# Performance work log

Hardware: AMD Instinct MI355X
Metric: run time of the kernel (lower is better)

The kernel has to match this reference:

```python
import jax, jax.numpy as jnp
import numpy as np

N, H, W, C = 4, 128, 128, 128
G = 8
GC = C // G
K = 9  # 3x3 deformable kernel
PAD = 1
HIN, WIN = H + 2 * PAD, W + 2 * PAD
EPS = 1e-5
OFFSET_SCALE = 1.0


def ln(x, g, b):
    m = jnp.mean(x, -1, keepdims=True)
    v = jnp.mean((x - m) ** 2, -1, keepdims=True)
    return (x - m) * jax.lax.rsqrt(v + EPS) * g + b


def gelu(x):
    return jax.nn.gelu(x, approximate=False)


def dcn_core(xp, offset, mask):
    # xp: (N,H,W,C) value features; offset: (N,H,W,G*K*2); mask: (N,H,W,G,K)
    xpad = jnp.pad(xp, ((0, 0), (PAD, PAD), (PAD, PAD), (0, 0)))
    img = xpad.reshape(N, HIN * WIN, G, GC)
    # reference points normalized by padded size (matches dcnv3_core_pytorch)
    ref_x = (jnp.arange(W, dtype=jnp.float32) + 1.5) / WIN  # (dil*(k-1))//2 + 0.5
    ref_y = (jnp.arange(H, dtype=jnp.float32) + 1.5) / HIN
    RX, RY = jnp.meshgrid(ref_x, ref_y)  # (H,W), xy indexing
    ref = jnp.stack([RX, RY], -1)  # (H,W,2) as (x,y)
    gx, gy = jnp.meshgrid(jnp.linspace(-1.0, 1.0, 3), jnp.linspace(-1.0, 1.0, 3), indexing='ij')
    grid = jnp.stack([gx / WIN, gy / HIN], -1).reshape(K, 2)  # dilation grid, x-major
    off = offset.reshape(N, H, W, G, K, 2)
    loc = (ref[None, :, :, None, None, :] + grid * OFFSET_SCALE
           + off * OFFSET_SCALE / jnp.array([WIN, HIN], jnp.float32))  # (N,H,W,G,K,2)
    # grid_sample align_corners=False pixel coords
    px = loc[..., 0] * WIN - 0.5
    py = loc[..., 1] * HIN - 0.5
    x0 = jnp.floor(px); y0 = jnp.floor(py)
    tx = px - x0; ty = py - y0
    x0i = x0.astype(jnp.int32); y0i = y0.astype(jnp.int32)
    x1i = x0i + 1; y1i = y0i + 1

    def gather(iy, ix):
        valid = ((iy >= 0) & (iy < HIN) & (ix >= 0) & (ix < WIN)).astype(xp.dtype)
        idx = jnp.clip(iy, 0, HIN - 1) * WIN + jnp.clip(ix, 0, WIN - 1)  # (N,H,W,G,K)
        idxf = idx.transpose(0, 1, 2, 4, 3).reshape(N, H * W * K, G, 1)
        v = jnp.take_along_axis(img, idxf, axis=1).reshape(N, H, W, K, G, GC)
        return v * valid.transpose(0, 1, 2, 4, 3)[..., None]

    acc = jnp.zeros((N, H, W, G, GC), xp.dtype)
    for iy, ix, wgt in ((y0i, x0i, (1 - ty) * (1 - tx)),
                        (y0i, x1i, (1 - ty) * tx),
                        (y1i, x0i, ty * (1 - tx)),
                        (y1i, x1i, ty * tx)):
        wm = (wgt * mask).transpose(0, 1, 2, 4, 3)[..., None]  # (N,H,W,K,G,1)
        acc = acc + jnp.sum(gather(iy, ix) * wm, axis=3)  # (N,H,W,G,GC)
    return acc.reshape(N, H, W, C)


def dcn(x, in_w, in_b, dw_k, dw_b, dwln_g, dwln_b, off_w, off_b, mask_w, mask_b, out_w, out_b):
    xp = x @ in_w + in_b  # input_proj
    # offset/mask branch: depthwise 3x3 conv on raw input, LN, GELU
    xc = jax.lax.conv_general_dilated(
        x, dw_k.reshape(3, 3, 1, C), (1, 1), 'SAME',
        dimension_numbers=('NHWC', 'HWIO', 'NHWC'), feature_group_count=C) + dw_b
    x1 = gelu(ln(xc, dwln_g, dwln_b))
    offset = x1 @ off_w + off_b  # (N,H,W,G*K*2)
    mask = jax.nn.softmax((x1 @ mask_w + mask_b).reshape(N, H, W, G, K), axis=-1)
    y = dcn_core(xp, offset, mask)
    return y @ out_w + out_b


def _forward(x, ln1_g, ln1_b, in_w, in_b, dw_k, dw_b, dwln_g, dwln_b, off_w, off_b,
             mask_w, mask_b, out_w, out_b, ln2_g, ln2_b, fc1_w, fc1_b, fc2_w, fc2_b):
    # pre-norm, no layer_scale, no drop_path (rate 0)
    x = x + dcn(ln(x, ln1_g, ln1_b), in_w, in_b, dw_k, dw_b, dwln_g, dwln_b,
                off_w, off_b, mask_w, mask_b, out_w, out_b)
    h = ln(x, ln2_g, ln2_b)
    h = gelu(h @ fc1_w + fc1_b) @ fc2_w + fc2_b
    return x + h


def setup_inputs() -> dict:
    key = jax.random.key(0)
    ks = jax.random.split(key, 10)

    def lin(k, fin, fout, scale=1.0):
        s = scale / np.sqrt(fin)
        return jax.random.uniform(k, (fin, fout), minval=-s, maxval=s, dtype=jnp.float32)

    d = {}
    d['x'] = jax.random.normal(ks[0], (N, H, W, C), dtype=jnp.float32)
    d['ln1_g'] = jnp.ones((C,), jnp.float32); d['ln1_b'] = jnp.zeros((C,), jnp.float32)
    d['in_w'] = lin(ks[1], C, C); d['in_b'] = jnp.zeros((C,), jnp.float32)
    d['dw_k'] = jax.random.normal(ks[2], (3, 3, C), dtype=jnp.float32) * 0.05
    d['dw_b'] = jnp.zeros((C,), jnp.float32)
    d['dwln_g'] = jnp.ones((C,), jnp.float32); d['dwln_b'] = jnp.zeros((C,), jnp.float32)
    d['off_w'] = lin(ks[3], C, G * K * 2, 0.1); d['off_b'] = jnp.zeros((G * K * 2,), jnp.float32)
    d['mask_w'] = lin(ks[4], C, G * K, 0.1); d['mask_b'] = jnp.zeros((G * K,), jnp.float32)
    d['out_w'] = lin(ks[5], C, C); d['out_b'] = jnp.zeros((C,), jnp.float32)
    d['ln2_g'] = jnp.ones((C,), jnp.float32); d['ln2_b'] = jnp.zeros((C,), jnp.float32)
    d['fc1_w'] = lin(ks[6], C, 4 * C); d['fc1_b'] = jnp.zeros((4 * C,), jnp.float32)
    d['fc2_w'] = lin(ks[7], 4 * C, C); d['fc2_b'] = jnp.zeros((C,), jnp.float32)
    return d


def reference(x, ln1_g, ln1_b, in_w, in_b, dw_k, dw_b, dwln_g, dwln_b, off_w, off_b,
              mask_w, mask_b, out_w, out_b, ln2_g, ln2_b, fc1_w, fc1_b, fc2_w, fc2_b):
    return _forward(x, ln1_g, ln1_b, in_w, in_b, dw_k, dw_b, dwln_g, dwln_b, off_w, off_b,
                    mask_w, mask_b, out_w, out_b, ln2_g, ln2_b, fc1_w, fc1_b, fc2_w, fc2_b)
```

## Files before the change

kernel.cpp:

```cpp
#include <hip/hip_runtime.h>
#include <hip/hip_bf16.h>
#include <math.h>

#define NB 4
#define HH 128
#define WW 128
#define CC 128
#define GG 8
#define GCC 16
#define KK 9
#define NHW (NB*HH*WW)

typedef __hip_bfloat16 bf16;
typedef __attribute__((ext_vector_type(8))) short short8;
typedef __attribute__((ext_vector_type(4))) float f32x4;

__device__ __forceinline__ float b2f(bf16 v){ return __bfloat162float(v); }
__device__ __forceinline__ bf16 f2b(float v){ return __float2bfloat16(v); }
__device__ __forceinline__ float gelu_f(float v){ return 0.5f*v*(1.f+erff(v*0.70710678118654752f)); }
__device__ __forceinline__ float lo_bf(unsigned u){ union{unsigned i; float f;} c; c.i = u<<16; return c.f; }
__device__ __forceinline__ float hi_bf(unsigned u){ union{unsigned i; float f;} c; c.i = u&0xffff0000u; return c.f; }
__device__ __forceinline__ unsigned pk(float a, float b){
  return ((unsigned)__bfloat16_as_ushort(f2b(b))<<16) | (unsigned)__bfloat16_as_ushort(f2b(a));
}
__device__ __forceinline__ void st_out(bf16* p, float v){ *p = f2b(v); }
__device__ __forceinline__ void st_out(float* p, float v){ *p = v; }
__device__ __forceinline__ void acc8(float* a, uint4 u, float w){
  a[0]+=w*lo_bf(u.x); a[1]+=w*hi_bf(u.x); a[2]+=w*lo_bf(u.y); a[3]+=w*hi_bf(u.y);
  a[4]+=w*lo_bf(u.z); a[5]+=w*hi_bf(u.z); a[6]+=w*lo_bf(u.w); a[7]+=w*hi_bf(u.w);
}

__global__ __launch_bounds__(256) void prep_k(
    const float* __restrict__ inw,  const float* __restrict__ outw,
    const float* __restrict__ fc1w, const float* __restrict__ fc2w,
    const float* __restrict__ offw, const float* __restrict__ offb,
    const float* __restrict__ maskw,const float* __restrict__ maskb,
    bf16* __restrict__ inwt, bf16* __restrict__ outwt,
    bf16* __restrict__ w1t,  bf16* __restrict__ w2t,
    bf16* __restrict__ wsw,  float* __restrict__ cw)
{
  int idx = blockIdx.x*256 + threadIdx.x;
  if (idx < 16384){
    int n = idx>>7, k = idx&127;
    inwt[idx] = f2b(inw[(size_t)k*128 + n]);
  } else if (idx < 32768){
    int i = idx-16384; int n = i>>7, k = i&127;
    outwt[i] = f2b(outw[(size_t)k*128 + n]);
  } else if (idx < 98304){
    int i = idx-32768; int n = i>>7, k = i&127;
    w1t[i] = f2b(fc1w[(size_t)k*512 + n]);
  } else if (idx < 163840){
    int i = idx-98304; int n = i>>9, k = i&511;
    w2t[i] = f2b(fc2w[(size_t)k*128 + n]);
  } else if (idx < 192512){
    int i = idx-163840; int nn = i>>7, k = i&127;
    float v = (nn<144) ? offw[(size_t)k*144+nn] : (nn<216 ? maskw[(size_t)k*72+(nn-144)] : 0.f);
    wsw[i] = f2b(v);
  } else if (idx < 192736){
    int i = idx-192512;
    cw[i] = (i<144) ? offb[i] : (i<216 ? maskb[i-144] : 0.f);
  }
}

__global__ __launch_bounds__(256) void ln_k(const float* __restrict__ X,
    const float* __restrict__ gam, const float* __restrict__ bet, bf16* __restrict__ Y)
{
  int lane = threadIdx.x & 63;
  int wid  = threadIdx.x >> 6;
  size_t pix = (size_t)blockIdx.x*4 + wid;
  const float* xp = X + pix*CC;
  int c0 = lane*2;
  float v0 = xp[c0], v1 = xp[c0+1];
  float s = v0+v1, ss = v0*v0+v1*v1;
  #pragma unroll
  for (int off=32; off>0; off>>=1){ s += __shfl_xor(s,off,64); ss += __shfl_xor(ss,off,64); }
  float mean = s*(1.f/CC);
  float var  = ss*(1.f/CC) - mean*mean;
  float rstd = rsqrtf(var + 1e-5f);
  float y0 = (v0-mean)*rstd*gam[c0]   + bet[c0];
  float y1 = (v1-mean)*rstd*gam[c0+1] + bet[c0+1];
  Y[pix*CC + c0]   = f2b(y0);
  Y[pix*CC + c0+1] = f2b(y1);
}

__global__ __launch_bounds__(256) void convln_k(const bf16* __restrict__ XN,
    const float* __restrict__ dwk, const float* __restrict__ dwb,
    const float* __restrict__ gam, const float* __restrict__ bet, bf16* __restrict__ X1)
{
  int tid = threadIdx.x;
  int px = tid>>4, cg = tid&15;
  int ch0 = cg*8;
  int pix = blockIdx.x*16 + px;
  int w = pix & (WW-1), h = (pix>>7)&(HH-1), n = pix>>14;
  float acc[8];
  {
    float4 b0 = *(const float4*)(dwb + ch0), b1 = *(const float4*)(dwb + ch0 + 4);
    acc[0]=b0.x; acc[1]=b0.y; acc[2]=b0.z; acc[3]=b0.w;
    acc[4]=b1.x; acc[5]=b1.y; acc[6]=b1.z; acc[7]=b1.w;
  }
  #pragma unroll
  for (int ky=0;ky<3;ky++){
    int yy = h+ky-1; if ((unsigned)yy>=(unsigned)HH) continue;
    #pragma unroll
    for (int kx=0;kx<3;kx++){
      int xx = w+kx-1; if ((unsigned)xx>=(unsigned)WW) continue;
      uint4 u = *(const uint4*)(XN + ((size_t)((n*HH+yy)*WW+xx))*CC + ch0);
      const float* wp = dwk + (ky*3+kx)*CC + ch0;
      float4 w0 = *(const float4*)wp; float4 w1 = *(const float4*)(wp+4);
      acc[0] += lo_bf(u.x)*w0.x; acc[1] += hi_bf(u.x)*w0.y;
      acc[2] += lo_bf(u.y)*w0.z; acc[3] += hi_bf(u.y)*w0.w;
      acc[4] += lo_bf(u.z)*w1.x; acc[5] += hi_bf(u.z)*w1.y;
      acc[6] += lo_bf(u.w)*w1.z; acc[7] += hi_bf(u.w)*w1.w;
    }
  }
  float s=0.f, ss=0.f;
  #pragma unroll
  for (int i=0;i<8;i++){ s += acc[i]; ss += acc[i]*acc[i]; }
  #pragma unroll
  for (int off=1; off<16; off<<=1){ s += __shfl_xor(s,off,64); ss += __shfl_xor(ss,off,64); }
  float mean=s*(1.f/CC), var=ss*(1.f/CC)-mean*mean, rstd=rsqrtf(var+1e-5f);
  float4 g0 = *(const float4*)(gam + ch0), g1 = *(const float4*)(gam + ch0 + 4);
  float4 be0 = *(const float4*)(bet + ch0), be1 = *(const float4*)(bet + ch0 + 4);
  float gv[8] = {g0.x,g0.y,g0.z,g0.w,g1.x,g1.y,g1.z,g1.w};
  float bv[8] = {be0.x,be0.y,be0.z,be0.w,be1.x,be1.y,be1.z,be1.w};
  float o[8];
  #pragma unroll
  for (int i=0;i<8;i++) o[i] = gelu_f((acc[i]-mean)*rstd*gv[i] + bv[i]);
  uint4 up; up.x = pk(o[0],o[1]); up.y = pk(o[2],o[3]); up.z = pk(o[4],o[5]); up.w = pk(o[6],o[7]);
  *(uint4*)(X1 + (size_t)pix*CC + ch0) = up;
}

#define OMS 226
__global__ __launch_bounds__(256) void samp_k(const bf16* __restrict__ X1,
    const bf16* __restrict__ XP,
    const bf16* __restrict__ wsw, const float* __restrict__ cw,
    bf16* __restrict__ Y)
{
  __shared__ bf16 oms[32*OMS];
  int tid = threadIdx.x;
  int pix0 = blockIdx.x*32;
  int wave = tid>>6, l = tid&63, lo16 = l&15, quad = l>>4;
  int nt0 = wave*4;
  int ntn = (wave==3) ? 2 : 4;
  short8 af[2][4];
  #pragma unroll
  for (int mt=0;mt<2;mt++)
    #pragma unroll
    for (int ks=0;ks<4;ks++)
      af[mt][ks] = *(const short8*)(X1 + (size_t)(pix0+mt*16+lo16)*128 + ks*32 + quad*8);
  f32x4 z = {0.f,0.f,0.f,0.f};
  f32x4 acc[2][4];
  #pragma unroll
  for (int mt=0;mt<2;mt++)
    #pragma unroll
    for (int t=0;t<4;t++) acc[mt][t]=z;
  for (int t=0;t<ntn;t++){
    int nt = nt0+t;
    #pragma unroll
    for (int ks=0;ks<4;ks++){
      short8 bfr = *(const short8*)(wsw + (size_t)(nt*16+lo16)*128 + ks*32 + quad*8);
      acc[0][t] = __builtin_amdgcn_mfma_f32_16x16x32_bf16(af[0][ks], bfr, acc[0][t], 0,0,0);
      acc[1][t] = __builtin_amdgcn_mfma_f32_16x16x32_bf16(af[1][ks], bfr, acc[1][t], 0,0,0);
    }
  }
  for (int t=0;t<ntn;t++){
    int col = (nt0+t)*16 + lo16;
    float bb = cw[col];
    #pragma unroll
    for (int mt=0;mt<2;mt++)
      #pragma unroll
      for (int r=0;r<4;r++)
        oms[(mt*16 + quad*4 + r)*OMS + col] = f2b(acc[mt][t][r] + bb);
  }
  __syncthreads();
  {
    int m = tid>>3, g = tid&7;
    int base = m*OMS + 144 + g*9;
    float sc[9]; float mx = -1e30f;
    #pragma unroll
    for (int k=0;k<9;k++){ sc[k] = b2f(oms[base+k]); mx = fmaxf(mx, sc[k]); }
    float sum = 0.f;
    #pragma unroll
    for (int k=0;k<9;k++){ sc[k] = expf(sc[k]-mx); sum += sc[k]; }
    float inv = 1.f/sum;
    #pragma unroll
    for (int k=0;k<9;k++) oms[base+k] = f2b(sc[k]*inv);
  }
  __syncthreads();
  int oct = tid&15, sl = tid>>4;
  int g = oct>>1;
  int ch = g*GCC + (oct&1)*8;
  int w0 = pix0 & (WW-1);
  int h  = (pix0>>7) & (HH-1);
  int n  = pix0>>14;
  const bf16* base = XP + (size_t)n*HH*WW*CC + ch;
  for (int it=0; it<2; it++){
    int m = it*16 + sl;
    int wc = w0 + m;
    const bf16* omrow = &oms[m*OMS];
    float a[8] = {0.f,0.f,0.f,0.f,0.f,0.f,0.f,0.f};
    #pragma unroll
    for (int k=0;k<9;k++){
      float offx = b2f(omrow[g*18 + 2*k]);
      float offy = b2f(omrow[g*18 + 2*k + 1]);
      float mk   = b2f(omrow[144 + g*9 + k]);
      float pxf = (float)(wc + (k/3) - 1) + offx;
      float pyf = (float)(h  + (k%3) - 1) + offy;
      float x0f = floorf(pxf), y0f = floorf(pyf);
      float txf = pxf-x0f,     tyf = pyf-y0f;
      int x0 = (int)x0f, y0 = (int)y0f;
      int x1i = x0+1,    y1i = y0+1;
      float vx0 = ((unsigned)x0 <(unsigned)WW)?1.f:0.f;
      float vx1 = ((unsigned)x1i<(unsigned)WW)?1.f:0.f;
      float vy0 = ((unsigned)y0 <(unsigned)HH)?1.f:0.f;
      float vy1 = ((unsigned)y1i<(unsigned)HH)?1.f:0.f;
      int cx0 = min(max(x0,0),WW-1),  cx1 = min(max(x1i,0),WW-1);
      int cy0 = min(max(y0,0),HH-1),  cy1 = min(max(y1i,0),HH-1);
      float w00=(1.f-tyf)*(1.f-txf)*mk*vy0*vx0, w01=(1.f-tyf)*txf*mk*vy0*vx1;
      float w10=tyf*(1.f-txf)*mk*vy1*vx0,       w11=tyf*txf*mk*vy1*vx1;
      uint4 u00 = *(const uint4*)(base + ((size_t)(cy0*WW+cx0))*CC);
      uint4 u01 = *(const uint4*)(base + ((size_t)(cy0*WW+cx1))*CC);
      uint4 u10 = *(const uint4*)(base + ((size_t)(cy1*WW+cx0))*CC);
      uint4 u11 = *(const uint4*)(base + ((size_t)(cy1*WW+cx1))*CC);
      acc8(a,u00,w00); acc8(a,u01,w01); acc8(a,u10,w10); acc8(a,u11,w11);
    }
    uint4 outp;
    outp.x = pk(a[0],a[1]); outp.y = pk(a[2],a[3]);
    outp.z = pk(a[4],a[5]); outp.w = pk(a[6],a[7]);
    *(uint4*)(Y + (size_t)(pix0+m)*CC + ch) = outp;
  }
}

template<typename OutT, bool RES>
__global__ __launch_bounds__(256) void gemm_mfma(const bf16* __restrict__ A,
    const bf16* __restrict__ Bt, const float* __restrict__ bias,
    const float* __restrict__ res, OutT* __restrict__ C)
{
  int tid = threadIdx.x;
  int wave = tid>>6, l = tid&63, lo16 = l&15, quad = l>>4;
  int m0 = blockIdx.y*256 + wave*64;
  int n0 = blockIdx.x*64;
  short8 bfr[4][4];
  #pragma unroll
  for (int ks=0;ks<4;ks++)
    #pragma unroll
    for (int nt=0;nt<4;nt++)
      bfr[ks][nt] = *(const short8*)(Bt + (size_t)(n0+nt*16+lo16)*128 + ks*32 + quad*8);
  f32x4 z = {0.f,0.f,0.f,0.f};
  f32x4 acc[4][4];
  #pragma unroll
  for (int mt=0;mt<4;mt++)
    #pragma unroll
    for (int nt=0;nt<4;nt++) acc[mt][nt]=z;
  #pragma unroll
  for (int ks=0;ks<4;ks++){
    short8 af[4];
    #pragma unroll
    for (int mt=0;mt<4;mt++)
      af[mt] = *(const short8*)(A + (size_t)(m0+mt*16+lo16)*128 + ks*32 + quad*8);
    #pragma unroll
    for (int nt=0;nt<4;nt++)
      #pragma unroll
      for (int mt=0;mt<4;mt++)
        acc[mt][nt] = __builtin_amdgcn_mfma_f32_16x16x32_bf16(af[mt], bfr[ks][nt], acc[mt][nt], 0,0,0);
  }
  #pragma unroll
  for (int mt=0;mt<4;mt++)
    #pragma unroll
    for (int nt=0;nt<4;nt++){
      int col = n0 + nt*16 + lo16;
      float bb = bias[col];
      #pragma unroll
      for (int r=0;r<4;r++){
        int row = m0 + mt*16 + quad*4 + r;
        float v = acc[mt][nt][r] + bb;
        if (RES) v += res[(size_t)row*128 + col];
        st_out(&C[(size_t)row*128 + col], v);
      }
    }
}

__global__ __launch_bounds__(256) void mlp_mfma(const float* __restrict__ X2,
    const float* __restrict__ lng, const float* __restrict__ lnb,
    const bf16* __restrict__ w1t, const float* __restrict__ b1,
    const bf16* __restrict__ w2t, const float* __restrict__ b2,
    float* __restrict__ OUT)
{
  __shared__ __align__(16) char smem[34816 + 18432];
  bf16* h0s = (bf16*)smem;
  bf16* ts  = (bf16*)smem;
  bf16* w1s = (bf16*)(smem + 34816);
  bf16* w2s = (bf16*)(smem + 34816);
  int tid = threadIdx.x;
  int wave = tid>>6, l = tid&63, lo16 = l&15, quad = l>>4;
  int m0 = blockIdx.x*128;
  #pragma unroll
  for (int itn=0; itn<2; itn++){
    int px = (tid>>2) + itn*64;
    int q = tid&3;
    const float* xr = X2 + (size_t)(m0+px)*128 + q*32;
    float v[32];
    #pragma unroll
    for (int i=0;i<8;i++) *(float4*)(v+i*4) = *(const float4*)(xr+i*4);
    float s=0.f, ss=0.f;
    #pragma unroll
    for (int i=0;i<32;i++){ s += v[i]; ss += v[i]*v[i]; }
    s  += __shfl_xor(s,1,64);  ss += __shfl_xor(ss,1,64);
    s  += __shfl_xor(s,2,64);  ss += __shfl_xor(ss,2,64);
    float mean = s*(1.f/CC), var = ss*(1.f/CC)-mean*mean, rstd = rsqrtf(var+1e-5f);
    const float* gp = lng + q*32; const float* bp = lnb + q*32;
    uint4* dst = (uint4*)(&h0s[px*136 + q*32]);
    #pragma unroll
    for (int i=0;i<4;i++){
      float4 g0 = *(const float4*)(gp+i*8),  g1 = *(const float4*)(gp+i*8+4);
      float4 c0v = *(const float4*)(bp+i*8), c1v = *(const float4*)(bp+i*8+4);
      float o0 = (v[i*8+0]-mean)*rstd*g0.x + c0v.x;
      float o1 = (v[i*8+1]-mean)*rstd*g0.y + c0v.y;
      float o2 = (v[i*8+2]-mean)*rstd*g0.z + c0v.z;
      float o3 = (v[i*8+3]-mean)*rstd*g0.w + c0v.w;
      float o4 = (v[i*8+4]-mean)*rstd*g1.x + c1v.x;
      float o5 = (v[i*8+5]-mean)*rstd*g1.y + c1v.y;
      float o6 = (v[i*8+6]-mean)*rstd*g1.z + c1v.z;
      float o7 = (v[i*8+7]-mean)*rstd*g1.w + c1v.w;
      uint4 up; up.x = pk(o0,o1); up.y = pk(o2,o3); up.z = pk(o4,o5); up.w = pk(o6,o7);
      dst[i] = up;
    }
  }
  __syncthreads();
  short8 a1[2][4];
  #pragma unroll
  for (int mt=0;mt<2;mt++)
    #pragma unroll
    for (int ks=0;ks<4;ks++)
      a1[mt][ks] = *(const short8*)(&h0s[(wave*32 + mt*16 + lo16)*136 + ks*32 + quad*8]);
  f32x4 z = {0.f,0.f,0.f,0.f};
  f32x4 acc2[2][8];
  #pragma unroll
  for (int mt=0;mt<2;mt++)
    #pragma unroll
    for (int nt=0;nt<8;nt++) acc2[mt][nt]=z;

  for (int c0=0;c0<512;c0+=64){
    __syncthreads();
    #pragma unroll
    for (int it=0;it<4;it++){
      int e = it*2048 + tid*8;
      int nn = e>>7, kk = e&127;
      *(uint4*)(&w1s[nn*136 + kk]) = *(const uint4*)(w1t + (size_t)(c0+nn)*128 + kk);
    }
    __syncthreads();
    f32x4 acc1[2][4];
    #pragma unroll
    for (int mt=0;mt<2;mt++)
      #pragma unroll
      for (int nt=0;nt<4;nt++) acc1[mt][nt]=z;
    #pragma unroll
    for (int ks=0;ks<4;ks++)
      #pragma unroll
      for (int nt=0;nt<4;nt++){
        short8 bfr = *(const short8*)(&w1s[(nt*16+lo16)*136 + ks*32 + quad*8]);
        acc1[0][nt] = __builtin_amdgcn_mfma_f32_16x16x32_bf16(a1[0][ks], bfr, acc1[0][nt], 0,0,0);
        acc1[1][nt] = __builtin_amdgcn_mfma_f32_16x16x32_bf16(a1[1][ks], bfr, acc1[1][nt], 0,0,0);
      }
    #pragma unroll
    for (int mt=0;mt<2;mt++)
      #pragma unroll
      for (int nt=0;nt<4;nt++){
        float bb = b1[c0 + nt*16 + lo16];
        #pragma unroll
        for (int r=0;r<4;r++)
          ts[(wave*32 + mt*16 + quad*4 + r)*72 + nt*16 + lo16] = f2b(gelu_f(acc1[mt][nt][r] + bb));
      }
    __syncthreads();
    #pragma unroll
    for (int it=0;it<4;it++){
      int e = it*2048 + tid*8;
      int nn = e>>6, kk = e&63;
      *(uint4*)(&w2s[nn*72 + kk]) = *(const uint4*)(w2t + (size_t)nn*512 + c0 + kk);
    }
    __syncthreads();
    #pragma unroll
    for (int ks2=0;ks2<2;ks2++){
      short8 a2[2];
      #pragma unroll
      for (int mt=0;mt<2;mt++)
        a2[mt] = *(const short8*)(&ts[(wave*32 + mt*16 + lo16)*72 + ks2*32 + quad*8]);
      #pragma unroll
      for (int nt2=0;nt2<8;nt2++){
        short8 bfr2 = *(const short8*)(&w2s[(nt2*16+lo16)*72 + ks2*32 + quad*8]);
        acc2[0][nt2] = __builtin_amdgcn_mfma_f32_16x16x32_bf16(a2[0], bfr2, acc2[0][nt2], 0,0,0);
        acc2[1][nt2] = __builtin_amdgcn_mfma_f32_16x16x32_bf16(a2[1], bfr2, acc2[1][nt2], 0,0,0);
      }
    }
  }
  #pragma unroll
  for (int mt=0;mt<2;mt++)
    #pragma unroll
    for (int nt=0;nt<8;nt++){
      int col = nt*16 + lo16;
      float bb = b2[col];
      #pragma unroll
      for (int r=0;r<4;r++){
        int row = m0 + wave*32 + mt*16 + quad*4 + r;
        float v = acc2[mt][nt][r] + bb + X2[(size_t)row*128 + col];
        OUT[(size_t)row*128 + col] = v;
      }
    }
}

extern "C" void kernel_launch(void* const* d_in, const int* in_sizes, int n_in,
                              void* d_out, int out_size, void* d_ws, size_t ws_size,
                              hipStream_t stream)
{
  const float* x    = (const float*)d_in[0];
  const float* ln1g = (const float*)d_in[1];
  const float* ln1b = (const float*)d_in[2];
  const float* inw  = (const float*)d_in[3];
  const float* inb  = (const float*)d_in[4];
  const float* dwk  = (const float*)d_in[5];
  const float* dwb  = (const float*)d_in[6];
  const float* dwlng= (const float*)d_in[7];
  const float* dwlnb= (const float*)d_in[8];
  const float* offw = (const float*)d_in[9];
  const float* offb = (const float*)d_in[10];
  const float* maskw= (const float*)d_in[11];
  const float* maskb= (const float*)d_in[12];
  const float* outw = (const float*)d_in[13];
  const float* outb = (const float*)d_in[14];
  const float* ln2g = (const float*)d_in[15];
  const float* ln2b = (const float*)d_in[16];
  const float* fc1w = (const float*)d_in[17];
  const float* fc1b = (const float*)d_in[18];
  const float* fc2w = (const float*)d_in[19];
  const float* fc2b = (const float*)d_in[20];
  float* out = (float*)d_out;

  bf16* ws = (bf16*)d_ws;
  const size_t S = (size_t)NHW*CC;
  bf16* xn = ws;
  bf16* xp = ws + S;
  bf16* x1 = ws + 2*S;
  bf16* y  = xn;
  float* x2 = out;
  bf16* inwt  = ws + 3*S;
  bf16* outwt = inwt + 128*128;
  bf16* w1t   = outwt + 128*128;
  bf16* w2t   = w1t + 512*128;
  bf16* wsw   = w2t + 128*512;
  float* cw   = (float*)(wsw + 224*128);

  prep_k<<<753, 256, 0, stream>>>(inw, outw, fc1w, fc2w, offw, offb, maskw, maskb,
                                  inwt, outwt, w1t, w2t, wsw, cw);
  ln_k<<<NHW/4, 256, 0, stream>>>(x, ln1g, ln1b, xn);
  gemm_mfma<bf16,false><<<dim3(2,256), 256, 0, stream>>>(xn, inwt, inb, nullptr, xp);
  convln_k<<<NHW/16, 256, 0, stream>>>(xn, dwk, dwb, dwlng, dwlnb, x1);
  samp_k<<<NHW/32, 256, 0, stream>>>(x1, xp, wsw, cw, y);
  gemm_mfma<float,true><<<dim3(2,256), 256, 0, stream>>>(y, outwt, outb, x, x2);
  mlp_mfma<<<NHW/128, 256, 0, stream>>>(x2, ln2g, ln2b, w1t, fc1b, w2t, fc2b, out);
}
```

Before: 282.8 us.

## Fuse LN1 with input projection; halve MLP tile and merge weight-load barriers

Replaces the separate LayerNorm kernel and input-projection GEMM with one kernel. It normalizes a 64-pixel tile into shared memory, writes the bf16 result to global for the conv path, and runs the MFMA projection from LDS, which removes one launch and a global re-read of xn. The MLP kernel now uses 64-row tiles instead of 128, doubling the grid to 1024 blocks. It also gives fc1 and fc2 weights separate LDS buffers so both load behind a single barrier per chunk. Smaller tiles mean each block reuses the weights it loads across fewer rows, so weight traffic from L2 goes up in exchange for better occupancy and parallelism.

```diff
diff --git a/kernel.cpp b/kernel.cpp
--- a/kernel.cpp
+++ b/kernel.cpp
@@ -62,25 +62,84 @@
   }
 }
 
-__global__ __launch_bounds__(256) void ln_k(const float* __restrict__ X,
-    const float* __restrict__ gam, const float* __restrict__ bet, bf16* __restrict__ Y)
-{
-  int lane = threadIdx.x & 63;
-  int wid  = threadIdx.x >> 6;
-  size_t pix = (size_t)blockIdx.x*4 + wid;
-  const float* xp = X + pix*CC;
-  int c0 = lane*2;
-  float v0 = xp[c0], v1 = xp[c0+1];
-  float s = v0+v1, ss = v0*v0+v1*v1;
-  #pragma unroll
-  for (int off=32; off>0; off>>=1){ s += __shfl_xor(s,off,64); ss += __shfl_xor(ss,off,64); }
-  float mean = s*(1.f/CC);
-  float var  = ss*(1.f/CC) - mean*mean;
-  float rstd = rsqrtf(var + 1e-5f);
-  float y0 = (v0-mean)*rstd*gam[c0]   + bet[c0];
-  float y1 = (v1-mean)*rstd*gam[c0+1] + bet[c0+1];
-  Y[pix*CC + c0]   = f2b(y0);
-  Y[pix*CC + c0+1] = f2b(y1);
+__global__ __launch_bounds__(256) void lnproj_k(const float* __restrict__ X,
+    const float* __restrict__ lng, const float* __restrict__ lnb,
+    const bf16* __restrict__ inwt, const float* __restrict__ inb,
+    bf16* __restrict__ XN, bf16* __restrict__ XP)
+{
+  __shared__ bf16 h0s[64*136];
+  __shared__ bf16 wst[64*136];
+  int tid = threadIdx.x;
+  int wave = tid>>6, l = tid&63, lo16 = l&15, quad = l>>4;
+  int m0 = blockIdx.x*64;
+  {
+    int px = tid>>2, q = tid&3;
+    const float* xr = X + (size_t)(m0+px)*128 + q*32;
+    float v[32];
+    #pragma unroll
+    for (int i=0;i<8;i++) *(float4*)(v+i*4) = *(const float4*)(xr+i*4);
+    float s=0.f, ss=0.f;
+    #pragma unroll
+    for (int i=0;i<32;i++){ s += v[i]; ss += v[i]*v[i]; }
+    s  += __shfl_xor(s,1,64);  ss += __shfl_xor(ss,1,64);
+    s  += __shfl_xor(s,2,64);  ss += __shfl_xor(ss,2,64);
+    float mean = s*(1.f/CC), var = ss*(1.f/CC)-mean*mean, rstd = rsqrtf(var+1e-5f);
+    const float* gp = lng + q*32; const float* bp = lnb + q*32;
+    uint4* dst  = (uint4*)(&h0s[px*136 + q*32]);
+    uint4* dstg = (uint4*)(XN + (size_t)(m0+px)*128 + q*32);
+    #pragma unroll
+    for (int i=0;i<4;i++){
+      float4 g0 = *(const float4*)(gp+i*8),  g1 = *(const float4*)(gp+i*8+4);
+      float4 c0v = *(const float4*)(bp+i*8), c1v = *(const float4*)(bp+i*8+4);
+      float o0 = (v[i*8+0]-mean)*rstd*g0.x + c0v.x;
+      float o1 = (v[i*8+1]-mean)*rstd*g0.y + c0v.y;
+      float o2 = (v[i*8+2]-mean)*rstd*g0.z + c0v.z;
+      float o3 = (v[i*8+3]-mean)*rstd*g0.w + c0v.w;
+      float o4 = (v[i*8+4]-mean)*rstd*g1.x + c1v.x;
+      float o5 = (v[i*8+5]-mean)*rstd*g1.y + c1v.y;
+      float o6 = (v[i*8+6]-mean)*rstd*g1.z + c1v.z;
+      float o7 = (v[i*8+7]-mean)*rstd*g1.w + c1v.w;
+      uint4 up; up.x = pk(o0,o1); up.y = pk(o2,o3); up.z = pk(o4,o5); up.w = pk(o6,o7);
+      dst[i] = up; dstg[i] = up;
+    }
+  }
+  __syncthreads();
+  short8 a1[4];
+  #pragma unroll
+  for (int ks=0;ks<4;ks++)
+    a1[ks] = *(const short8*)(&h0s[(wave*16+lo16)*136 + ks*32 + quad*8]);
+  f32x4 z = {0.f,0.f,0.f,0.f};
+  #pragma unroll
+  for (int nc=0;nc<2;nc++){
+    if (nc) __syncthreads();
+    #pragma unroll
+    for (int it=0;it<4;it++){
+      int e = it*2048 + tid*8;
+      int nn = e>>7, kk = e&127;
+      *(uint4*)(&wst[nn*136 + kk]) = *(const uint4*)(inwt + (size_t)(nc*64+nn)*128 + kk);
+    }
+    __syncthreads();
+    f32x4 acc[4];
+    #pragma unroll
+    for (int nt=0;nt<4;nt++) acc[nt]=z;
+    #pragma unroll
+    for (int ks=0;ks<4;ks++)
+      #pragma unroll
+      for (int nt=0;nt<4;nt++){
+        short8 bfr = *(const short8*)(&wst[(nt*16+lo16)*136 + ks*32 + quad*8]);
+        acc[nt] = __builtin_amdgcn_mfma_f32_16x16x32_bf16(a1[ks], bfr, acc[nt], 0,0,0);
+      }
+    #pragma unroll
+    for (int nt=0;nt<4;nt++){
+      int col = nc*64 + nt*16 + lo16;
+      float bb = inb[col];
+      #pragma unroll
+      for (int r=0;r<4;r++){
+        int row = m0 + wave*16 + quad*4 + r;
+        XP[(size_t)row*128 + col] = f2b(acc[nt][r] + bb);
+      }
+    }
+  }
 }
 
 __global__ __launch_bounds__(256) void convln_k(const bf16* __restrict__ XN,
@@ -286,18 +345,16 @@
     const bf16* __restrict__ w2t, const float* __restrict__ b2,
     float* __restrict__ OUT)
 {
-  __shared__ __align__(16) char smem[34816 + 18432];
+  __shared__ __align__(16) char smem[17408 + 17408 + 18432];
   bf16* h0s = (bf16*)smem;
   bf16* ts  = (bf16*)smem;
-  bf16* w1s = (bf16*)(smem + 34816);
+  bf16* w1s = (bf16*)(smem + 17408);
   bf16* w2s = (bf16*)(smem + 34816);
   int tid = threadIdx.x;
   int wave = tid>>6, l = tid&63, lo16 = l&15, quad = l>>4;
-  int m0 = blockIdx.x*128;
-  #pragma unroll
-  for (int itn=0; itn<2; itn++){
-    int px = (tid>>2) + itn*64;
-    int q = tid&3;
+  int m0 = blockIdx.x*64;
+  {
+    int px = tid>>2, q = tid&3;
     const float* xr = X2 + (size_t)(m0+px)*128 + q*32;
     float v[32];
     #pragma unroll
@@ -327,18 +384,14 @@
     }
   }
   __syncthreads();
-  short8 a1[2][4];
-  #pragma unroll
-  for (int mt=0;mt<2;mt++)
-    #pragma unroll
-    for (int ks=0;ks<4;ks++)
-      a1[mt][ks] = *(const short8*)(&h0s[(wave*32 + mt*16 + lo16)*136 + ks*32 + quad*8]);
+  short8 a1[4];
+  #pragma unroll
+  for (int ks=0;ks<4;ks++)
+    a1[ks] = *(const short8*)(&h0s[(wave*16+lo16)*136 + ks*32 + quad*8]);
   f32x4 z = {0.f,0.f,0.f,0.f};
-  f32x4 acc2[2][8];
-  #pragma unroll
-  for (int mt=0;mt<2;mt++)
-    #pragma unroll
-    for (int nt=0;nt<8;nt++) acc2[mt][nt]=z;
+  f32x4 acc2[8];
+  #pragma unroll
+  for (int nt=0;nt<8;nt++) acc2[nt]=z;
 
   for (int c0=0;c0<512;c0+=64){
     __syncthreads();
@@ -348,30 +401,6 @@
       int nn = e>>7, kk = e&127;
       *(uint4*)(&w1s[nn*136 + kk]) = *(const uint4*)(w1t + (size_t)(c0+nn)*128 + kk);
     }
-    __syncthreads();
-    f32x4 acc1[2][4];
-    #pragma unroll
-    for (int mt=0;mt<2;mt++)
-      #pragma unroll
-      for (int nt=0;nt<4;nt++) acc1[mt][nt]=z;
-    #pragma unroll
-    for (int ks=0;ks<4;ks++)
-      #pragma unroll
-      for (int nt=0;nt<4;nt++){
-        short8 bfr = *(const short8*)(&w1s[(nt*16+lo16)*136 + ks*32 + quad*8]);
-        acc1[0][nt] = __builtin_amdgcn_mfma_f32_16x16x32_bf16(a1[0][ks], bfr, acc1[0][nt], 0,0,0);
-        acc1[1][nt] = __builtin_amdgcn_mfma_f32_16x16x32_bf16(a1[1][ks], bfr, acc1[1][nt], 0,0,0);
-      }
-    #pragma unroll
-    for (int mt=0;mt<2;mt++)
-      #pragma unroll
-      for (int nt=0;nt<4;nt++){
-        float bb = b1[c0 + nt*16 + lo16];
-        #pragma unroll
-        for (int r=0;r<4;r++)
-          ts[(wave*32 + mt*16 + quad*4 + r)*72 + nt*16 + lo16] = f2b(gelu_f(acc1[mt][nt][r] + bb));
-      }
-    __syncthreads();
     #pragma unroll
     for (int it=0;it<4;it++){
       int e = it*2048 + tid*8;
@@ -379,33 +408,45 @@
       *(uint4*)(&w2s[nn*72 + kk]) = *(const uint4*)(w2t + (size_t)nn*512 + c0 + kk);
     }
     __syncthreads();
+    f32x4 acc1[4];
+    #pragma unroll
+    for (int nt=0;nt<4;nt++) acc1[nt]=z;
+    #pragma unroll
+    for (int ks=0;ks<4;ks++)
+      #pragma unroll
+      for (int nt=0;nt<4;nt++){
+        short8 bfr = *(const short8*)(&w1s[(nt*16+lo16)*136 + ks*32 + quad*8]);
+        acc1[nt] = __builtin_amdgcn_mfma_f32_16x16x32_bf16(a1[ks], bfr, acc1[nt], 0,0,0);
+      }
+    #pragma unroll
+    for (int nt=0;nt<4;nt++){
+      float bb = b1[c0 + nt*16 + lo16];
+      #pragma unroll
+      for (int r=0;r<4;r++)
+        ts[(wave*16 + quad*4 + r)*72 + nt*16 + lo16] = f2b(gelu_f(acc1[nt][r] + bb));
+    }
+    __syncthreads();
     #pragma unroll
     for (int ks2=0;ks2<2;ks2++){
-      short8 a2[2];
-      #pragma unroll
-      for (int mt=0;mt<2;mt++)
-        a2[mt] = *(const short8*)(&ts[(wave*32 + mt*16 + lo16)*72 + ks2*32 + quad*8]);
+      short8 a2 = *(const short8*)(&ts[(wave*16+lo16)*72 + ks2*32 + quad*8]);
       #pragma unroll
       for (int nt2=0;nt2<8;nt2++){
         short8 bfr2 = *(const short8*)(&w2s[(nt2*16+lo16)*72 + ks2*32 + quad*8]);
-        acc2[0][nt2] = __builtin_amdgcn_mfma_f32_16x16x32_bf16(a2[0], bfr2, acc2[0][nt2], 0,0,0);
-        acc2[1][nt2] = __builtin_amdgcn_mfma_f32_16x16x32_bf16(a2[1], bfr2, acc2[1][nt2], 0,0,0);
+        acc2[nt2] = __builtin_amdgcn_mfma_f32_16x16x32_bf16(a2, bfr2, acc2[nt2], 0,0,0);
       }
     }
   }
   #pragma unroll
-  for (int mt=0;mt<2;mt++)
-    #pragma unroll
-    for (int nt=0;nt<8;nt++){
-      int col = nt*16 + lo16;
-      float bb = b2[col];
-      #pragma unroll
-      for (int r=0;r<4;r++){
-        int row = m0 + wave*32 + mt*16 + quad*4 + r;
-        float v = acc2[mt][nt][r] + bb + X2[(size_t)row*128 + col];
-        OUT[(size_t)row*128 + col] = v;
-      }
-    }
+  for (int nt=0;nt<8;nt++){
+    int col = nt*16 + lo16;
+    float bb = b2[col];
+    #pragma unroll
+    for (int r=0;r<4;r++){
+      int row = m0 + wave*16 + quad*4 + r;
+      float v = acc2[nt][r] + bb + X2[(size_t)row*128 + col];
+      OUT[(size_t)row*128 + col] = v;
+    }
+  }
 }
 
 extern "C" void kernel_launch(void* const* d_in, const int* in_sizes, int n_in,
@@ -451,10 +492,9 @@
 
   prep_k<<<753, 256, 0, stream>>>(inw, outw, fc1w, fc2w, offw, offb, maskw, maskb,
                                   inwt, outwt, w1t, w2t, wsw, cw);
-  ln_k<<<NHW/4, 256, 0, stream>>>(x, ln1g, ln1b, xn);
-  gemm_mfma<bf16,false><<<dim3(2,256), 256, 0, stream>>>(xn, inwt, inb, nullptr, xp);
+  lnproj_k<<<NHW/64, 256, 0, stream>>>(x, ln1g, ln1b, inwt, inb, xn, xp);
   convln_k<<<NHW/16, 256, 0, stream>>>(xn, dwk, dwb, dwlng, dwlnb, x1);
   samp_k<<<NHW/32, 256, 0, stream>>>(x1, xp, wsw, cw, y);
   gemm_mfma<float,true><<<dim3(2,256), 256, 0, stream>>>(y, outwt, outb, x, x2);
-  mlp_mfma<<<NHW/128, 256, 0, stream>>>(x2, ln2g, ln2b, w1t, fc1b, w2t, fc2b, out);
-}
+  mlp_mfma<<<NHW/64, 256, 0, stream>>>(x2, ln2g, ln2b, w1t, fc1b, w2t, fc2b, out);
+}
```

New measurement: 292.9 us. 1.04x slower.
